# Performance work log

Hardware: AMD Instinct MI355X
Metric: run time of the kernel (lower is better)

Reference implementation:

```python
import jax, jax.numpy as jnp
import numpy as np

NEG = 0.2  # LeakyReLU slope

def lrelu(x):
    return jnp.where(x >= 0, x, NEG * x)

def conv2d(x, w, pad):
    return jax.lax.conv_general_dilated(x, w, (1, 1), [(pad, pad), (pad, pad)],
                                        dimension_numbers=('NCHW', 'OIHW', 'NCHW'))

def maxpool2(x):
    return jax.lax.reduce_window(x, -jnp.inf, jax.lax.max, (1, 1, 2, 2), (1, 1, 2, 2), 'VALID')

def batchnorm(x, g, b, eps=1e-5):
    m = jnp.mean(x, axis=(0, 2, 3), keepdims=True)
    v = jnp.var(x, axis=(0, 2, 3), keepdims=True)
    return (x - m) / jnp.sqrt(v + eps) * g[None, :, None, None] + b[None, :, None, None]

def features(x, cw1, bg1, bb1, cw2, bg2, bb2, cw3, bg3, bb3, cw4, bg4, bb4):
    x = maxpool2(lrelu(batchnorm(conv2d(x, cw1, 1), bg1, bb1)))
    x = maxpool2(lrelu(batchnorm(conv2d(x, cw2, 1), bg2, bb2)))
    x = lrelu(batchnorm(conv2d(x, cw3, 1), bg3, bb3))
    x = lrelu(batchnorm(conv2d(x, cw4, 1), bg4, bb4))
    return x  # [B,64,16,16]

def mhsa(x, wq, bq, wk, bk, wv, bv, rel_h, rel_w, ln_g, ln_b, heads=4):
    B, C, W, H = x.shape
    d, hw = C // heads, W * H
    def proj(w, b):
        return (jnp.einsum('oc,bchw->bohw', w, x) + b[None, :, None, None]).reshape(B, heads, d, hw)
    q, k, v = proj(wq, bq), proj(wk, bk), proj(wv, bv)
    cc = jnp.einsum('bhdi,bhdj->bhij', q, k)                 # content-content
    pos = (rel_h + rel_w).reshape(heads, d, hw)              # relative position bias
    cp = jnp.einsum('hdi,bhdj->bhij', pos, q)                # content-position
    attn = jax.nn.softmax(cc + cp, axis=-1)
    out = jnp.einsum('bhdj,bhij->bhdi', v, attn).reshape(B, C, W, H)
    m = jnp.mean(out, axis=(1, 2, 3), keepdims=True)
    va = jnp.var(out, axis=(1, 2, 3), keepdims=True)
    out = (out - m) / jnp.sqrt(va + 1e-5) * ln_g[None] + ln_b[None]
    return out + x

def cbam(x, cw1, cb1, cw2, cb2, sw, sb):
    avg, mx = jnp.mean(x, axis=(2, 3)), jnp.max(x, axis=(2, 3))
    def exc(f):
        return jnp.einsum('oc,bc->bo', cw2, jax.nn.relu(jnp.einsum('oc,bc->bo', cw1, f) + cb1)) + cb2
    x = jax.nn.sigmoid(exc(avg) + exc(mx))[:, :, None, None] * x
    sf = jnp.stack([jnp.mean(x, axis=1), jnp.max(x, axis=1)], axis=1)  # [B,2,H,W]
    sa = jax.nn.sigmoid(conv2d(sf, sw, 3) + sb[None, :, None, None])
    return sa * x

def sa_module(x, mh, cb):
    return mhsa(x, *mh) + cbam(x, *cb) + x

def setup_inputs() -> dict:
    key = jax.random.key(0)
    ks = jax.random.split(key, 24)
    rn = lambda k, s, sc=1.0: jax.random.normal(k, s, dtype=jnp.float32) * sc
    inp = {
        'input1': rn(ks[0], (64, 1, 64, 64)),
        'input2': rn(ks[1], (5, 5, 1, 64, 64)),
        'conv1_w': rn(ks[2], (64, 1, 3, 3), 0.3),
        'bn1_g': jnp.ones(64), 'bn1_b': jnp.zeros(64),
        'conv2_w': rn(ks[3], (64, 64, 3, 3), 0.05),
        'bn2_g': jnp.ones(64), 'bn2_b': jnp.zeros(64),
        'conv3_w': rn(ks[4], (64, 64, 3, 3), 0.05),
        'bn3_g': jnp.ones(64), 'bn3_b': jnp.zeros(64),
        'conv4_w': rn(ks[5], (64, 64, 3, 3), 0.05),
        'bn4_g': jnp.ones(64), 'bn4_b': jnp.zeros(64),
        'wq': rn(ks[6], (64, 64), 0.12), 'bq': rn(ks[7], (64,), 0.01),
        'wk': rn(ks[8], (64, 64), 0.12), 'bk': rn(ks[9], (64,), 0.01),
        'wv': rn(ks[10], (64, 64), 0.12), 'bv': rn(ks[11], (64,), 0.01),
        'rel_h': rn(ks[12], (1, 4, 16, 1, 16)),
        'rel_w': rn(ks[13], (1, 4, 16, 16, 1)),
        'ln_g': jnp.ones((64, 16, 16)), 'ln_b': jnp.zeros((64, 16, 16)),
        'ca_w1': rn(ks[14], (4, 64), 0.15), 'ca_b1': jnp.zeros(4),
        'ca_w2': rn(ks[15], (64, 4), 0.15), 'ca_b2': jnp.zeros(64),
        'sa_w': rn(ks[16], (1, 2, 7, 7), 0.1), 'sa_b': jnp.zeros(1),
        'cls_w': rn(ks[17], (256,), 0.05),
    }
    return inp

def reference(input1, input2, conv1_w, bn1_g, bn1_b, conv2_w, bn2_g, bn2_b,
              conv3_w, bn3_g, bn3_b, conv4_w, bn4_g, bn4_b,
              wq, bq, wk, bk, wv, bv, rel_h, rel_w, ln_g, ln_b,
              ca_w1, ca_b1, ca_w2, ca_b2, sa_w, sa_b, cls_w):
    fa = (conv1_w, bn1_g, bn1_b, conv2_w, bn2_g, bn2_b, conv3_w, bn3_g, bn3_b, conv4_w, bn4_g, bn4_b)
    mh = (wq, bq, wk, bk, wv, bv, rel_h, rel_w, ln_g, ln_b)
    cb = (ca_w1, ca_b1, ca_w2, ca_b2, sa_w, sa_b)
    q = sa_module(features(input1, *fa), mh, cb)                      # [B,64,16,16]
    S = jax.vmap(lambda imgs: sa_module(features(imgs, *fa), mh, cb))(input2)  # [ncls,shot,64,16,16]
    ncls, shot = input2.shape[0], input2.shape[1]
    B, C, Hh, Ww = q.shape
    hw = Hh * Ww
    # per-class covariance over channels (CovaBlock.cal_covariance)
    X = S.transpose(0, 2, 1, 3, 4).reshape(ncls, C, shot * hw)
    Xc = X - jnp.mean(X, axis=2, keepdims=True)
    cov = jnp.einsum('ncm,ndm->ncd', Xc, Xc) / (hw * shot - 1)        # [ncls,C,C]
    # query similarity: diag(q^T Cov q) done as fused quadratic form
    Q = q.reshape(B, C, hw)
    Qn = Q / jnp.linalg.norm(Q, axis=2, keepdims=True)
    sim = jnp.einsum('bci,jcd,bdi->bji', Qn, cov, Qn)                 # [B,ncls,hw]
    # classifier: LeakyReLU -> Dropout(eval=identity) -> Conv1d(k=hw, stride=hw, no bias)
    out = jnp.einsum('bjk,k->bj', lrelu(sim), cls_w)
    return out
```

## Files before the change

kernel.cpp:

```cpp
#include <hip/hip_runtime.h>
#include <hip/hip_bf16.h>

__device__ __forceinline__ float lrelu(float x){ return x >= 0.f ? x : 0.2f*x; }
__device__ __forceinline__ float sigm(float x){ return 1.f/(1.f+__expf(-x)); }

typedef short short8 __attribute__((ext_vector_type(8)));
typedef float f32x16 __attribute__((ext_vector_type(16)));

static constexpr size_t OFF_X0    = 0;
static constexpr size_t OFF_POS   = 475712;
static constexpr size_t OFF_WQT   = 492096;
static constexpr size_t OFF_STATS = 504384;
static constexpr size_t OFF_P1    = 507456;
static constexpr size_t OFF_P2    = 7092224;
static constexpr size_t OFF_S3    = 8937728;
static constexpr size_t OFF_S4    = 8943872;
static constexpr size_t OFF_WH3   = 8950016;
static constexpr size_t OFF_WL3   = 8968448;
static constexpr size_t OFF_WH4   = 8986880;
static constexpr size_t OFF_WL4   = 9005312;
static constexpr size_t OFF_S2    = 9023744;
static constexpr size_t OFF_RES   = 10714688;
static constexpr size_t OFF_MU    = 12172864;
static constexpr size_t OFF_COV   = 12173184;
static constexpr size_t OFF_SIM   = 12193664;
static constexpr size_t OFF_R1    = 12275584;
static constexpr size_t OFF_C2    = OFF_R1;
static constexpr size_t OFF_ATP   = OFF_R1;
static constexpr size_t OFF_C3    = OFF_R1 + 5832704;
static constexpr size_t OFF_C4    = OFF_R1 + 8749056;
static constexpr size_t OFF_CKV   = OFF_R1 + 10207232;
static constexpr size_t OFF_C3P   = OFF_R1 + 10207232;
static constexpr size_t OFF_QN    = OFF_R1 + 17543680;
static constexpr size_t OFF_WH    = OFF_R1 + 21737984;
static constexpr size_t OFF_WL    = OFF_WH + 18432;

__device__ __forceinline__ int bn_group(int img){ return (img < 64) ? 0 : (1 + (img-64)/5); }

__device__ __forceinline__ void bn_ab(const float* __restrict__ sums, int g, int c, float n,
                                      float gw, float bw, float& a, float& b)
{
    const float sum = sums[(g*64+c)*2], ss = sums[(g*64+c)*2+1];
    const float m = sum/n;
    const float var = fmaxf(ss/n - m*m, 0.f);
    const float istd = 1.f/sqrtf(var + 1e-5f);
    a = gw*istd;
    b = bw - m*a;
}

__device__ __forceinline__ void bn_ab_s8(const float* __restrict__ sums, int g, int c, float n,
                                         float gw, float bw, float& a, float& b)
{
    float sum = 0.f, ss = 0.f;
#pragma unroll
    for (int s=0;s<8;s++){
        sum += sums[s*768 + (g*64+c)*2];
        ss  += sums[s*768 + (g*64+c)*2 + 1];
    }
    const float m = sum/n;
    const float var = fmaxf(ss/n - m*m, 0.f);
    const float istd = 1.f/sqrtf(var + 1e-5f);
    a = gw*istd;
    b = bw - m*a;
}

__global__ __launch_bounds__(256) void prep_k(const float* __restrict__ in1, const float* __restrict__ in2,
        const float* __restrict__ relh, const float* __restrict__ relw,
        const float* __restrict__ wq, const float* __restrict__ wk, const float* __restrict__ wv,
        const float* __restrict__ cw2, const float* __restrict__ cw3, const float* __restrict__ cw4,
        float* __restrict__ ws)
{
    int idx = blockIdx.x*256 + threadIdx.x;
    if (idx < 364544) { ws[OFF_X0+idx] = (idx < 262144 ? in1[idx] : in2[idx-262144]); return; }
    idx -= 364544;
    if (idx < 16384) {
        const int h = idx>>12, r = idx&4095, i = r>>4, d = r&15;
        ws[OFF_POS+idx] = relh[h*256 + d*16 + (i&15)] + relw[h*256 + d*16 + (i>>4)];
        return;
    }
    idx -= 16384;
    if (idx < 12288) {
        const int s = idx/4096, r = idx%4096, c = r>>6, o = r&63;
        const float* wp = (s==0)?wq:((s==1)?wk:wv);
        ws[OFF_WQT+idx] = wp[o*64 + c];
        return;
    }
    idx -= 12288;
    if (idx < 3072) { ws[OFF_STATS+idx] = 0.f; return; }
    idx -= 3072;
    if (idx < 20480) { ws[OFF_COV+idx] = 0.f; return; }
    idx -= 20480;
    if (idx < 12288) { ws[OFF_S3+idx] = 0.f; return; }
    idx -= 12288;
    if (idx < 768) { ws[OFF_S2+idx] = 0.f; return; }
    idx -= 768;
    if (idx < 110592) {
        const int which = idx / 36864, r0 = idx - which*36864;
        const int och = r0/576, rr = r0%576, cin = rr/9, k9 = rr%9;
        const float* cwp = (which==0)?cw2:((which==1)?cw3:cw4);
        const float v = cwp[r0];
        __hip_bfloat16 hb = __float2bfloat16(v);
        const float hv = __bfloat162float(hb);
        __hip_bfloat16 lb = __float2bfloat16(v - hv);
        const size_t oh = (which==0)?OFF_WH:((which==1)?OFF_WH3:OFF_WH4);
        const size_t ol = (which==0)?OFF_WL:((which==1)?OFF_WL3:OFF_WL4);
        unsigned short* WH = (unsigned short*)(ws + oh);
        unsigned short* WL = (unsigned short*)(ws + ol);
        const int d = k9*4096 + och*64 + cin;
        WH[d] = *(unsigned short*)&hb;
        WL[d] = *(unsigned short*)&lb;
        return;
    }
    idx -= 110592;
    if (idx < 751872) {
        const int img = idx/8448, r = idx%8448;
        const int pos = r>>6, d = r&63;
        int ypad, xpad;
        if (pos < 68){ ypad = (pos<34)?0:33; xpad = (pos<34)?pos:(pos-34); }
        else { const int q = pos-68; ypad = 1 + (q>>1); xpad = (q&1)*33; }
        ws[OFF_P1 + (((size_t)img*34 + ypad)*34 + xpad)*64 + d] = 0.f;
        return;
    }
    idx -= 751872;
    if (idx < 387328) {
        const int img = idx/4352, r = idx%4352;
        const int pos = r>>6, d = r&63;
        int ypad, xpad;
        if (pos < 36){ ypad = (pos<18)?0:17; xpad = (pos<18)?pos:(pos-18); }
        else { const int q = pos-36; ypad = 1 + (q>>1); xpad = (q&1)*17; }
        ws[OFF_P2 + (((size_t)img*18 + ypad)*18 + xpad)*64 + d] = 0.f;
        return;
    }
    idx -= 387328;
    if (idx < 387328) {
        const int img = idx/4352, r = idx%4352;
        const int pos = r>>6, d = r&63;
        int ypad, xpad;
        if (pos < 36){ ypad = (pos<18)?0:17; xpad = (pos<18)?pos:(pos-18); }
        else { const int q = pos-36; ypad = 1 + (q>>1); xpad = (q&1)*17; }
        ws[OFF_C3P + (((size_t)img*18 + ypad)*18 + xpad)*64 + d] = 0.f;
    }
}

template<int H, int W, int CIN, int CH, int OCB, int PT, bool STORE, bool INBN>
__global__ __launch_bounds__(256) void conv3x3_k(const float* __restrict__ in,
                                                 const float* __restrict__ wt,
                                                 float* __restrict__ out,
                                                 float* __restrict__ bnsum,
                                                 const float* __restrict__ isums,
                                                 const float* __restrict__ igw,
                                                 const float* __restrict__ ibw,
                                                 int ihw)
{
    constexpr int P = W + 1;
    constexpr int PLANE = H * P;
    constexpr int HW = H * W;
    constexpr int PASSES = HW / (256 * PT);
    constexpr int NLD = CH * HW / 256;
    __shared__ float lds[CH * PLANE];
    __shared__ float redS[OCB*4], redQ[OCB*4];
    __shared__ float abA[64], abB[64];
    const int img = blockIdx.x;
    const int och0 = blockIdx.y * OCB;
    const int t = threadIdx.x;

    if constexpr (INBN) {
        if (t < CIN) {
            const int gi = bn_group(img);
            const float nin = (float)(((gi==0)?64:5) * ihw);
            float a, b;
            bn_ab(isums, gi, t, nin, igw[t], ibw[t], a, b);
            abA[t]=a; abB[t]=b;
        }
        __syncthreads();
    }

    float acc[PASSES][OCB][PT];
#pragma unroll
    for (int a=0;a<PASSES;a++)
#pragma unroll
      for (int o=0;o<OCB;o++)
#pragma unroll
        for (int p=0;p<PT;p++) acc[a][o][p]=0.f;

    for (int idx = t; idx < CH*HW; idx += 256) {
        const int c = idx / HW, p = idx % HW;
        float v = in[((size_t)img*CIN + c)*HW + p];
        if constexpr (INBN) v = lrelu(abA[c]*v + abB[c]);
        lds[c*PLANE + (p/W)*P + (p%W)] = v;
    }
    __syncthreads();

    for (int cc0 = 0; cc0 < CIN; cc0 += CH) {
        float pre[(CIN > CH) ? NLD : 1];
        if constexpr (CIN > CH) {
            if (cc0 + CH < CIN) {
#pragma unroll
                for (int j=0;j<NLD;j++){
                    const int idx = j*256 + t;
                    const int c = idx / HW, p = idx % HW;
                    pre[j] = in[((size_t)img*CIN + cc0 + CH + c)*HW + p];
                }
            }
        }
        for (int c = 0; c < CH; ++c) {
            float wr[OCB][9];
#pragma unroll
            for (int o=0;o<OCB;o++)
#pragma unroll
              for (int k=0;k<9;k++)
                wr[o][k] = wt[((size_t)(och0+o)*CIN + (cc0+c))*9 + k];
            const float* Lc = lds + c*PLANE;
#pragma unroll
            for (int ps=0; ps<PASSES; ++ps) {
                const int px0 = (ps*256 + t)*PT;
                const int y = px0 / W, x0 = px0 % W;
#pragma unroll
                for (int ky=0; ky<3; ++ky) {
                    const int yy = y + ky - 1;
                    if (yy >= 0 && yy < H) {
                        const float* Lr = Lc + yy*P;
                        float r[PT+2];
                        r[0] = (x0 > 0) ? Lr[x0-1] : 0.f;
#pragma unroll
                        for (int k2=0;k2<PT;k2++) r[k2+1] = Lr[x0+k2];
                        r[PT+1] = (x0+PT < W) ? Lr[x0+PT] : 0.f;
#pragma unroll
                        for (int p=0;p<PT;p++)
#pragma unroll
                          for (int kx=0;kx<3;kx++) {
                              const float v = r[p+kx];
#pragma unroll
                              for (int o=0;o<OCB;o++)
                                  acc[ps][o][p] += v * wr[o][ky*3+kx];
                          }
                    }
                }
            }
        }
        if constexpr (CIN > CH) {
            if (cc0 + CH < CIN) {
                __syncthreads();
#pragma unroll
                for (int j=0;j<NLD;j++){
                    const int idx = j*256 + t;
                    const int c = idx / HW, p = idx % HW;
                    float v = pre[j];
                    if constexpr (INBN) v = lrelu(abA[cc0+CH+c]*v + abB[cc0+CH+c]);
                    lds[c*PLANE + (p/W)*P + (p%W)] = v;
                }
                __syncthreads();
            }
        }
    }
    if constexpr (STORE) {
#pragma unroll
        for (int ps=0; ps<PASSES; ++ps) {
            const int px0 = (ps*256 + t)*PT;
#pragma unroll
            for (int o=0;o<OCB;o++)
#pragma unroll
              for (int p=0;p<PT;p++)
                out[((size_t)img*64 + och0+o)*HW + px0 + p] = acc[ps][o][p];
        }
    }
    const int g = bn_group(img);
    const int wv = t >> 6;
#pragma unroll
    for (int o=0;o<OCB;o++){
        float s=0.f, ss=0.f;
#pragma unroll
        for (int ps=0;ps<PASSES;ps++)
#pragma unroll
          for (int p=0;p<PT;p++){ const float v=acc[ps][o][p]; s+=v; ss+=v*v; }
#pragma unroll
        for (int off=32; off>0; off>>=1){ s += __shfl_xor(s, off); ss += __shfl_xor(ss, off); }
        if ((t&63)==0){ redS[o*4+wv]=s; redQ[o*4+wv]=ss; }
    }
    __syncthreads();
    if (t < OCB*2){
        const int o = t>>1, metric = t&1;
        const float v = metric ? (redQ[o*4]+redQ[o*4+1]+redQ[o*4+2]+redQ[o*4+3])
                               : (redS[o*4]+redS[o*4+1]+redS[o*4+2]+redS[o*4+3]);
        atomicAdd(&bnsum[(g*64 + och0+o)*2 + metric], v);
    }
}

__global__ __launch_bounds__(256) void bnpoolconv1_k(const float* __restrict__ x0,
        const float* __restrict__ cw, const float* __restrict__ sums,
        const float* __restrict__ gw, const float* __restrict__ bw,
        unsigned short* __restrict__ p1p)
{
    __shared__ float xl[10*64];
    __shared__ float wsm[576];
    __shared__ float aAs[64], aBs[64];
    const int img = blockIdx.x, band = blockIdx.y, t = threadIdx.x;
    const int oy0 = band*4;
    const float* xp = x0 + (size_t)img*4096;
    for (int idx=t; idx<640; idx+=256){
        const int iy = idx>>6, ix = idx&63;
        const int gy = 2*oy0 - 1 + iy;
        xl[idx] = (gy>=0 && gy<64) ? xp[gy*64+ix] : 0.f;
    }
    const int g = bn_group(img);
    if (t < 64){
        const float n = (float)(((g==0)?64:5) * 4096);
        float a, b;
        bn_ab(sums, g, t, n, gw[t], bw[t], a, b);
        aAs[t]=a; aBs[t]=b;
    }
    for (int idx=t; idx<576; idx+=256) wsm[idx] = cw[idx];
    __syncthreads();
    const int p = t>>1, half = t&1;
    const int ly = p>>5, ox = p&31;
    float r[4][4];
#pragma unroll
    for (int dy=0;dy<4;dy++){
        const float* Lr = xl + (2*ly+dy)*64;
#pragma unroll
        for (int dx=0;dx<4;dx++){
            const int xx = 2*ox-1+dx;
            r[dy][dx] = (xx>=0 && xx<64) ? Lr[xx] : 0.f;
        }
    }
    short8 hv[4], lv[4];
#pragma unroll
    for (int o=0;o<32;o++){
        const int och = half*32 + o;
        float w[9];
#pragma unroll
        for (int k=0;k<9;k++) w[k] = wsm[och*9+k];
        const float a = aAs[och], b = aBs[och];
        float best = -1e30f;
#pragma unroll
        for (int sy=0;sy<2;sy++)
#pragma unroll
          for (int sx=0;sx<2;sx++){
            float s=0.f;
#pragma unroll
            for (int ky=0;ky<3;ky++)
#pragma unroll
              for (int kx=0;kx<3;kx++) s += r[sy+ky][sx+kx]*w[ky*3+kx];
            best = fmaxf(best, lrelu(a*s+b));
          }
        __hip_bfloat16 hb = __float2bfloat16(best);
        const float hf = __bfloat162float(hb);
        __hip_bfloat16 lb = __float2bfloat16(best - hf);
        hv[o>>3][o&7] = (short)*(unsigned short*)&hb;
        lv[o>>3][o&7] = (short)*(unsigned short*)&lb;
    }
    const size_t base = ((((size_t)img*34 + (oy0+ly) + 1)*34) + ox + 1)*128 + half*32;
#pragma unroll
    for (int j=0;j<4;j++){
        *(short8*)(p1p + base + j*8)      = hv[j];
        *(short8*)(p1p + base + 64 + j*8) = lv[j];
    }
}

__global__ __launch_bounds__(256) void conv2mfma_k(const unsigned short* __restrict__ p1p,
        const unsigned short* __restrict__ whi, const unsigned short* __restrict__ wlo,
        float* __restrict__ c2)
{
    __shared__ __align__(16) unsigned short Bx[136*128];
    const int img = blockIdx.x, rowblk = blockIdx.y;
    const int t = threadIdx.x;
    {
        const unsigned short* src = p1p + (((size_t)img*34 + rowblk*2)*34)*128;
        for (int idx=t; idx<2176; idx+=256){
            const int pos = idx>>4, sub = idx&15;
            const short8 v = *(const short8*)(src + pos*128 + sub*8);
            *(short8*)(Bx + pos*128 + ((sub ^ (pos&15))<<3)) = v;
        }
    }
    __syncthreads();
    const int lane = t & 63, wv = t >> 6;
    const int mt = wv & 1, ntp = wv >> 1;
    const int m = lane & 31, kg = lane >> 5;
    f32x16 accA, accB, accC;
#pragma unroll
    for (int r=0;r<16;r++){ accA[r]=0.f; accB[r]=0.f; accC[r]=0.f; }

#pragma unroll
    for (int ky=0; ky<3; ky++){
#pragma unroll
      for (int kx=0; kx<3; kx++){
        const int s = ky*3 + kx;
        const unsigned short* wh = whi + ((s*64 + mt*32 + m)<<6) + kg*8;
        const unsigned short* wl = wlo + ((s*64 + mt*32 + m)<<6) + kg*8;
        const int pos = (ntp+ky)*34 + m + kx;
        const int pb  = pos << 7;
        const int sw  = (pos & 15) << 3;
#pragma unroll
        for (int ch=0; ch<4; ch++){
            const int o = ch*16 + (kg<<3);
            const short8 ah = *(const short8*)(wh + ch*16);
            const short8 al = *(const short8*)(wl + ch*16);
            const short8 bh = *(const short8*)(Bx + pb + (o ^ sw));
            const short8 bl = *(const short8*)(Bx + pb + ((64 + o) ^ sw));
            accA = __builtin_amdgcn_mfma_f32_32x32x16_bf16(ah, bh, accA, 0,0,0);
            accB = __builtin_amdgcn_mfma_f32_32x32x16_bf16(al, bh, accB, 0,0,0);
            accC = __builtin_amdgcn_mfma_f32_32x32x16_bf16(ah, bl, accC, 0,0,0);
        }
      }
    }
    const int py = rowblk*2 + ntp;
    float* co = c2 + (size_t)img*65536 + py*32 + m;
#pragma unroll
    for (int r=0; r<16; r++){
        const int och = mt*32 + (r&3) + 8*(r>>2) + 4*kg;
        co[(size_t)och*1024] = accA[r] + accB[r] + accC[r];
    }
}

__global__ __launch_bounds__(256) void bnstats2_k(const float* __restrict__ in, float* __restrict__ sums)
{
    __shared__ float rs[4], rq[4];
    const int img = blockIdx.x, c = blockIdx.y, t = threadIdx.x;
    const float4 v = ((const float4*)(in + ((size_t)img*64 + c)*1024))[t];
    float s = v.x+v.y+v.z+v.w;
    float q = v.x*v.x+v.y*v.y+v.z*v.z+v.w*v.w;
#pragma unroll
    for (int off=32; off>0; off>>=1){ s += __shfl_xor(s, off); q += __shfl_xor(q, off); }
    if ((t&63)==0){ rs[t>>6]=s; rq[t>>6]=q; }
    __syncthreads();
    if (t==0){
        const int g = bn_group(img);
        atomicAdd(&sums[(g*64+c)*2],   rs[0]+rs[1]+rs[2]+rs[3]);
        atomicAdd(&sums[(g*64+c)*2+1], rq[0]+rq[1]+rq[2]+rq[3]);
    }
}

__global__ __launch_bounds__(256) void bnpool_pack_k(const float* __restrict__ c2,
        const float* __restrict__ sums, const float* __restrict__ gw, const float* __restrict__ bw,
        unsigned short* __restrict__ p2p)
{
    __shared__ float aA[64], aB[64];
    const int img = blockIdx.x, cb = blockIdx.y, t = threadIdx.x;
    const int g = bn_group(img);
    if (t < 64){
        const float n = (float)(((g==0)?64:5) * 1024);
        float a, b;
        bn_ab(sums, g, t, n, gw[t], bw[t], a, b);
        aA[t]=a; aB[t]=b;
    }
    __syncthreads();
    const int oy = t>>4, ox = t&15;
    const float* pim = c2 + (size_t)img*65536 + (size_t)cb*32768 + oy*64 + ox*2;
    short8 hv[4], lv[4];
#pragma unroll
    for (int j8=0;j8<4;j8++){
#pragma unroll
      for (int e=0;e<8;e++){
        const int j = j8*8 + e;
        const int c = cb*32 + j;
        const float* pl = pim + (size_t)j*1024;
        const float2 u = *(const float2*)pl;
        const float2 v = *(const float2*)(pl + 32);
        const float a = aA[c], b = aB[c];
        const float best = fmaxf(fmaxf(lrelu(a*u.x+b), lrelu(a*u.y+b)),
                                 fmaxf(lrelu(a*v.x+b), lrelu(a*v.y+b)));
        __hip_bfloat16 hb = __float2bfloat16(best);
        const float hf = __bfloat162float(hb);
        __hip_bfloat16 lb = __float2bfloat16(best - hf);
        hv[j8][e] = (short)*(unsigned short*)&hb;
        lv[j8][e] = (short)*(unsigned short*)&lb;
      }
    }
    unsigned short* dst = p2p + (((size_t)img*18 + oy+1)*18 + ox+1)*128 + cb*32;
#pragma unroll
    for (int j=0;j<4;j++){
        *(short8*)(dst + j*8)      = hv[j];
        *(short8*)(dst + 64 + j*8) = lv[j];
    }
}

__global__ __launch_bounds__(256) void conv16mfma_k(const unsigned short* __restrict__ pack,
        const unsigned short* __restrict__ whi, const unsigned short* __restrict__ wlo,
        float* __restrict__ out, float* __restrict__ bnsum)
{
    __shared__ __align__(16) unsigned short Bx[108*128];
    const int img = blockIdx.x, rowblk = blockIdx.y;
    const int t = threadIdx.x;
    {
        const unsigned short* src = pack + (((size_t)img*18 + rowblk*4)*18)*128;
        for (int idx=t; idx<1728; idx+=256){
            const int pos = idx>>4, sub = idx&15;
            const short8 v = *(const short8*)(src + pos*128 + sub*8);
            *(short8*)(Bx + pos*128 + ((sub ^ (pos&15))<<3)) = v;
        }
    }
    __syncthreads();
    const int lane = t & 63, wv = t >> 6;
    const int mt = wv & 1, np = wv >> 1;
    const int m = lane & 31, kg = lane >> 5;
    f32x16 accA, accB, accC;
#pragma unroll
    for (int r=0;r<16;r++){ accA[r]=0.f; accB[r]=0.f; accC[r]=0.f; }

#pragma unroll
    for (int ky=0; ky<3; ky++){
#pragma unroll
      for (int kx=0; kx<3; kx++){
        const int s = ky*3 + kx;
        const unsigned short* wh = whi + ((s*64 + mt*32 + m)<<6) + kg*8;
        const unsigned short* wl = wlo + ((s*64 + mt*32 + m)<<6) + kg*8;
        const int pos = (np*2 + (m>>4) + ky)*18 + (m&15) + kx;
        const int pb  = pos << 7;
        const int sw  = (pos & 15) << 3;
#pragma unroll
        for (int ch=0; ch<4; ch++){
            const int o = ch*16 + (kg<<3);
            const short8 ah = *(const short8*)(wh + ch*16);
            const short8 al = *(const short8*)(wl + ch*16);
            const short8 bh = *(const short8*)(Bx + pb + (o ^ sw));
            const short8 bl = *(const short8*)(Bx + pb + ((64 + o) ^ sw));
            accA = __builtin_amdgcn_mfma_f32_32x32x16_bf16(ah, bh, accA, 0,0,0);
            accB = __builtin_amdgcn_mfma_f32_32x32x16_bf16(al, bh, accB, 0,0,0);
            accC = __builtin_amdgcn_mfma_f32_32x32x16_bf16(ah, bl, accC, 0,0,0);
        }
      }
    }
    float* co = out + (size_t)img*16384 + rowblk*64 + np*32 + m;
    float fa[16];
#pragma unroll
    for (int r=0; r<16; r++){
        fa[r] = accA[r] + accB[r] + accC[r];
        const int och = mt*32 + (r&3) + 8*(r>>2) + 4*kg;
        co[(size_t)och*256] = fa[r];
    }
    const int g = bn_group(img);
    float* bs = bnsum + (rowblk*2 + np)*768;
#pragma unroll
    for (int r=0; r<16; r++){
        float sv = fa[r], qv = fa[r]*fa[r];
#pragma unroll
        for (int off=16; off>0; off>>=1){ sv += __shfl_xor(sv, off); qv += __shfl_xor(qv, off); }
        if (m == r){
            const int och = mt*32 + (r&3) + 8*(r>>2) + 4*kg;
            atomicAdd(&bs[(g*64+och)*2],   sv);
            atomicAdd(&bs[(g*64+och)*2+1], qv);
        }
    }
}

__global__ __launch_bounds__(256) void c3pack_k(const float* __restrict__ c3,
        const float* __restrict__ s3, const float* __restrict__ gw, const float* __restrict__ bw,
        unsigned short* __restrict__ c3p)
{
    __shared__ float aA[64], aB[64];
    const int img = blockIdx.x, cb = blockIdx.y, t = threadIdx.x;
    const int g = bn_group(img);
    if (t < 64){
        const float n = (float)(((g==0)?64:5) * 256);
        float a, b;
        bn_ab_s8(s3, g, t, n, gw[t], bw[t], a, b);
        aA[t]=a; aB[t]=b;
    }
    __syncthreads();
    const float* pim = c3 + (size_t)img*16384 + (size_t)cb*8192 + t;
    short8 hv[4], lv[4];
#pragma unroll
    for (int j8=0;j8<4;j8++){
#pragma unroll
      for (int e=0;e<8;e++){
        const int j = j8*8 + e;
        const int c = cb*32 + j;
        const float v = lrelu(aA[c]*pim[(size_t)j*256] + aB[c]);
        __hip_bfloat16 hb = __float2bfloat16(v);
        const float hf = __bfloat162float(hb);
        __hip_bfloat16 lb = __float2bfloat16(v - hf);
        hv[j8][e] = (short)*(unsigned short*)&hb;
        lv[j8][e] = (short)*(unsigned short*)&lb;
      }
    }
    const int oy = t>>4, ox = t&15;
    unsigned short* dst = c3p + (((size_t)img*18 + oy+1)*18 + ox+1)*128 + cb*32;
#pragma unroll
    for (int j=0;j<4;j++){
        *(short8*)(dst + j*8)      = hv[j];
        *(short8*)(dst + 64 + j*8) = lv[j];
    }
}

__global__ __launch_bounds__(256) void proj_k(const float* __restrict__ c4, const float* __restrict__ wT,
               const float* __restrict__ bq, const float* __restrict__ bk, const float* __restrict__ bv,
               const float* __restrict__ sums4, const float* __restrict__ gw4, const float* __restrict__ bw4,
               float* __restrict__ ckv)
{
    __shared__ float xl[64*256];
    const int img = blockIdx.x, s = blockIdx.y, t = threadIdx.x;
    const int gi = bn_group(img);
    const float nin = (float)(((gi==0)?64:5) * 256);
    {
        const float4* in4 = (const float4*)(c4 + (size_t)img*16384);
        float4* xl4 = (float4*)xl;
        for (int i=t; i<4096; i+=256){
            float4 v = in4[i];
            const int c = i>>6;
            float a, b;
            bn_ab_s8(sums4, gi, c, nin, gw4[c], bw4[c], a, b);
            v.x=lrelu(a*v.x+b); v.y=lrelu(a*v.y+b); v.z=lrelu(a*v.z+b); v.w=lrelu(a*v.w+b);
            xl4[i] = v;
        }
    }
    const float* bias = (s==0)?bq:((s==1)?bk:bv);
    const int sofs = (s==0)?16:((s==1)?0:32);
    const float* wp = wT + s*4096;
    const int o0 = (t>>4)*4, i0 = (t&15)*16;
    const int h = o0>>4, d0 = o0&15;
    __syncthreads();
    float acc[4][16];
    float b0[4];
#pragma unroll
// ... 205 lines not shown
#pragma unroll 4
        for (int cc=0; cc<16; ++cc){
            const int c = cb*16 + cc;
            const int i4 = c*64 + q;
            const float4 mv = *(const float4*)&mh_l[c*256 + q*4];
            const float4 fv = fb4[i4], gv = lg4[i4], bv = lb4[i4];
            const float a = aA[c], b = aB[c], cf = ca[c];
            float4 r;
            r.x = (mv.x-m)*istd*gv.x + bv.x + lrelu(a*fv.x+b)*(2.f + sa0*cf);
            r.y = (mv.y-m)*istd*gv.y + bv.y + lrelu(a*fv.y+b)*(2.f + sa1*cf);
            r.z = (mv.z-m)*istd*gv.z + bv.z + lrelu(a*fv.z+b)*(2.f + sa2*cf);
            r.w = (mv.w-m)*istd*gv.w + bv.w + lrelu(a*fv.w+b)*(2.f + sa3*cf);
            res4[i4] = r;
        }
    }
}

__global__ __launch_bounds__(256) void covmu_k(const float* __restrict__ res, float* __restrict__ mu)
{
    __shared__ float r1[256];
    const int n = blockIdx.x, c = blockIdx.y, t = threadIdx.x;
    float s=0.f;
    for (int sh=0; sh<5; ++sh)
        s += res[((size_t)(64 + n*5 + sh)*64 + c)*256 + t];
    r1[t]=s; __syncthreads();
    for (int st=128;st>0;st>>=1){ if(t<st) r1[t]+=r1[t+st]; __syncthreads(); }
    if (t==0) mu[n*64+c] = r1[0]/1280.f;
}

__global__ __launch_bounds__(256) void cov_k(const float* __restrict__ res, const float* __restrict__ mu,
                                             float* __restrict__ cov)
{
    __shared__ float Xl[64*129];
    const int n = blockIdx.x, by = blockIdx.y, sh = blockIdx.z, t = threadIdx.x;
    const int c = by*16 + (t>>4);
    const int d0 = (t&15)*4;
    float acc[4] = {0.f,0.f,0.f,0.f};
    for (int half=0; half<2; ++half){
        __syncthreads();
        for (int idx=t; idx<8192; idx+=256){
            const int ch = idx>>7, p = idx&127;
            Xl[ch*129+p] = res[((size_t)(64+n*5+sh)*64 + ch)*256 + half*128 + p] - mu[n*64+ch];
        }
        __syncthreads();
        for (int p=0;p<128;p++){
            const float xc = Xl[c*129+p];
#pragma unroll
            for (int k=0;k<4;k++) acc[k] += xc*Xl[(d0+k)*129+p];
        }
    }
#pragma unroll
    for (int k=0;k<4;k++) atomicAdd(&cov[((size_t)n*64 + c)*64 + d0+k], acc[k]*(1.f/1279.f));
}

__global__ __launch_bounds__(64) void qn_k(const float* __restrict__ res, float* __restrict__ qn)
{
    const int b = blockIdx.x, c = blockIdx.y, t = threadIdx.x;
    const size_t base = ((size_t)b*64 + c)*256;
    const float4 v = *(const float4*)(res + base + t*4);
    float ss = v.x*v.x + v.y*v.y + v.z*v.z + v.w*v.w;
#pragma unroll
    for (int off=32; off>0; off>>=1) ss += __shfl_xor(ss, off);
    const float inv = 1.f/sqrtf(ss);
    float4 o; o.x=v.x*inv; o.y=v.y*inv; o.z=v.z*inv; o.w=v.w*inv;
    *(float4*)(qn + base + t*4) = o;
}

__global__ __launch_bounds__(256) void sim_k(const float* __restrict__ qn, const float* __restrict__ cov,
                                             float* __restrict__ sim)
{
    __shared__ float covj[64*65];
    __shared__ float Vl[64*68];
    __shared__ float simred[320];
    const int b = blockIdx.x, iq = blockIdx.y, t = threadIdx.x;
    const int i0g = iq*64;
    for (int idx=t; idx<4096; idx+=256){
        const int c = idx>>6, il = idx&63;
        Vl[c*68+il] = qn[((size_t)b*64+c)*256 + i0g + il];
    }
    for (int idx=t; idx<320; idx+=256) simred[idx]=0.f;
    const int c0 = (t>>4)*4, i0 = (t&15)*4;
    for (int j=0;j<5;j++){
        __syncthreads();
        for (int idx=t; idx<4096; idx+=256)
            covj[(idx>>6)*65 + (idx&63)] = cov[(size_t)j*4096 + idx];
        __syncthreads();
        float pt[4][4];
#pragma unroll
        for (int a=0;a<4;a++)
#pragma unroll
          for (int bb=0;bb<4;bb++) pt[a][bb]=0.f;
        for (int d=0; d<64; ++d){
            const float4 vv = *(const float4*)&Vl[d*68 + i0];
            float cw[4];
#pragma unroll
            for (int cc=0;cc<4;cc++) cw[cc] = covj[(c0+cc)*65 + d];
#pragma unroll
            for (int cc=0;cc<4;cc++){
                pt[cc][0] += cw[cc]*vv.x;
                pt[cc][1] += cw[cc]*vv.y;
                pt[cc][2] += cw[cc]*vv.z;
                pt[cc][3] += cw[cc]*vv.w;
            }
        }
#pragma unroll
        for (int ii=0;ii<4;ii++){
            float s = 0.f;
#pragma unroll
            for (int cc=0;cc<4;cc++) s += pt[cc][ii]*Vl[(c0+cc)*68 + i0+ii];
            atomicAdd(&simred[j*64 + i0 + ii], s);
        }
    }
    __syncthreads();
    for (int idx=t; idx<320; idx+=256){
        const int j = idx>>6, il = idx&63;
        sim[((size_t)b*5 + j)*256 + i0g + il] = simred[idx];
    }
}

__global__ __launch_bounds__(256) void cls_k(const float* __restrict__ sim, const float* __restrict__ cw,
                                             float* __restrict__ out)
{
    __shared__ float red[256];
    const int b = blockIdx.x, t = threadIdx.x;
    const float w = cw[t];
    for (int j=0;j<5;j++){
        const float v = sim[((size_t)b*5 + j)*256 + t];
        red[t] = lrelu(v)*w;
        __syncthreads();
        for (int st=128;st>0;st>>=1){ if(t<st) red[t]+=red[t+st]; __syncthreads(); }
        if (t==0) out[b*5+j] = red[0];
        __syncthreads();
    }
}

extern "C" void kernel_launch(void* const* d_in, const int* in_sizes, int n_in,
                              void* d_out, int out_size, void* d_ws, size_t ws_size,
                              hipStream_t stream)
{
    const float* IN[31];
    for (int i=0;i<31;i++) IN[i] = (const float*)d_in[i];
    float* W = (float*)d_ws;
    float* OUT = (float*)d_out;
    const unsigned short* WHp  = (const unsigned short*)(W + OFF_WH);
    const unsigned short* WLp  = (const unsigned short*)(W + OFF_WL);
    const unsigned short* WH3p = (const unsigned short*)(W + OFF_WH3);
    const unsigned short* WL3p = (const unsigned short*)(W + OFF_WL3);
    const unsigned short* WH4p = (const unsigned short*)(W + OFF_WH4);
    const unsigned short* WL4p = (const unsigned short*)(W + OFF_WL4);
    unsigned short* P1P = (unsigned short*)(W + OFF_P1);
    unsigned short* P2P = (unsigned short*)(W + OFF_P2);
    unsigned short* C3P = (unsigned short*)(W + OFF_C3P);

    prep_k<<<8074,256,0,stream>>>(IN[0],IN[1],IN[20],IN[21],IN[14],IN[16],IN[18],
                                  IN[5],IN[8],IN[11],W);

    conv3x3_k<64,64,1,1,4,4,false,false><<<dim3(89,16),256,0,stream>>>(W+OFF_X0, IN[2], nullptr, W+OFF_STATS, nullptr,nullptr,nullptr,0);
    bnpoolconv1_k<<<dim3(89,8),256,0,stream>>>(W+OFF_X0, IN[2], W+OFF_STATS, IN[3], IN[4], P1P);

    conv2mfma_k<<<dim3(89,16),256,0,stream>>>(P1P, WHp, WLp, W+OFF_C2);
    bnstats2_k<<<dim3(89,64),256,0,stream>>>(W+OFF_C2, W+OFF_S2);
    bnpool_pack_k<<<dim3(89,2),256,0,stream>>>(W+OFF_C2, W+OFF_S2, IN[6], IN[7], P2P);

    conv16mfma_k<<<dim3(89,4),256,0,stream>>>(P2P, WH3p, WL3p, W+OFF_C3, W+OFF_S3);
    c3pack_k<<<dim3(89,2),256,0,stream>>>(W+OFF_C3, W+OFF_S3, IN[9], IN[10], C3P);

    conv16mfma_k<<<dim3(89,4),256,0,stream>>>(C3P, WH4p, WL4p, W+OFF_C4, W+OFF_S4);

    proj_k<<<dim3(89,3),256,0,stream>>>(W+OFF_C4, W+OFF_WQT, IN[15], IN[17], IN[19],
                                        W+OFF_S4, IN[12], IN[13], W+OFF_CKV);
    attnp_k<<<dim3(89,4,4),256,0,stream>>>(W+OFF_CKV, W+OFF_POS, W+OFF_ATP);

    post_k<<<89,256,0,stream>>>(W+OFF_ATP, IN[22], IN[23], W+OFF_C4,
                                W+OFF_S4, IN[12], IN[13],
                                IN[24], IN[25], IN[26], IN[27], IN[28], IN[29], W+OFF_RES);

    covmu_k<<<dim3(5,64),256,0,stream>>>(W+OFF_RES, W+OFF_MU);
    cov_k<<<dim3(5,4,5),256,0,stream>>>(W+OFF_RES, W+OFF_MU, W+OFF_COV);
    qn_k<<<dim3(64,64),64,0,stream>>>(W+OFF_RES, W+OFF_QN);
    sim_k<<<dim3(64,4),256,0,stream>>>(W+OFF_QN, W+OFF_COV, W+OFF_SIM);
    cls_k<<<64,256,0,stream>>>(W+OFF_SIM, IN[30], OUT);
}
```

Before: 512.1 us.

## Fuse conv2 BN statistics and 2x2 max/min pooling into the MFMA conv epilogue

The conv2 MFMA kernel now reduces per-channel sum and sum-of-squares with wave shuffles and atomics into 32 slot-partitioned accumulators. It also pools 2x2 windows into max and min buffers, so the full 32x32 conv2 output is never written to global memory. The separate bnstats2 kernel is removed. bnpool_pack picks max or min depending on the sign of the BN scale, which stays exact because lrelu is monotone. This removes a large intermediate write and read plus a launch, at the cost of more atomics and extra epilogue work in the conv kernel.

```diff
diff --git a/kernel.cpp b/kernel.cpp
--- a/kernel.cpp
+++ b/kernel.cpp
@@ -25,7 +25,8 @@
 static constexpr size_t OFF_COV   = 12173184;
 static constexpr size_t OFF_SIM   = 12193664;
 static constexpr size_t OFF_R1    = 12275584;
-static constexpr size_t OFF_C2    = OFF_R1;
+static constexpr size_t OFF_PMAX  = OFF_R1;
+static constexpr size_t OFF_PMIN  = OFF_R1 + 1458176;
 static constexpr size_t OFF_ATP   = OFF_R1;
 static constexpr size_t OFF_C3    = OFF_R1 + 5832704;
 static constexpr size_t OFF_C4    = OFF_R1 + 8749056;
@@ -64,6 +65,22 @@
     b = bw - m*a;
 }
 
+__device__ __forceinline__ void bn_ab_s32(const float* __restrict__ sums, int g, int c, float n,
+                                          float gw, float bw, float& a, float& b)
+{
+    float sum = 0.f, ss = 0.f;
+#pragma unroll
+    for (int s=0;s<32;s++){
+        sum += sums[s*768 + (g*64+c)*2];
+        ss  += sums[s*768 + (g*64+c)*2 + 1];
+    }
+    const float m = sum/n;
+    const float var = fmaxf(ss/n - m*m, 0.f);
+    const float istd = 1.f/sqrtf(var + 1e-5f);
+    a = gw*istd;
+    b = bw - m*a;
+}
+
 __global__ __launch_bounds__(256) void prep_k(const float* __restrict__ in1, const float* __restrict__ in2,
         const float* __restrict__ relh, const float* __restrict__ relw,
         const float* __restrict__ wq, const float* __restrict__ wk, const float* __restrict__ wv,
@@ -92,8 +109,8 @@
     idx -= 20480;
     if (idx < 12288) { ws[OFF_S3+idx] = 0.f; return; }
     idx -= 12288;
-    if (idx < 768) { ws[OFF_S2+idx] = 0.f; return; }
-    idx -= 768;
+    if (idx < 24576) { ws[OFF_S2+idx] = 0.f; return; }
+    idx -= 24576;
     if (idx < 110592) {
         const int which = idx / 36864, r0 = idx - which*36864;
         const int och = r0/576, rr = r0%576, cin = rr/9, k9 = rr%9;
@@ -359,7 +376,7 @@
 
 __global__ __launch_bounds__(256) void conv2mfma_k(const unsigned short* __restrict__ p1p,
         const unsigned short* __restrict__ whi, const unsigned short* __restrict__ wlo,
-        float* __restrict__ c2)
+        float* __restrict__ pmax, float* __restrict__ pmin, float* __restrict__ bnsum)
 {
     __shared__ __align__(16) unsigned short Bx[136*128];
     const int img = blockIdx.x, rowblk = blockIdx.y;
@@ -403,34 +420,54 @@
         }
       }
     }
-    const int py = rowblk*2 + ntp;
-    float* co = c2 + (size_t)img*65536 + py*32 + m;
+    float fa[16];
+#pragma unroll
+    for (int r=0;r<16;r++) fa[r] = accA[r] + accB[r] + accC[r];
+
+    const int g = bn_group(img);
+    float* bs = bnsum + (rowblk*2 + ntp)*768;
+#pragma unroll
+    for (int r=0; r<16; r++){
+        float sv = fa[r], qv = fa[r]*fa[r];
+#pragma unroll
+        for (int off=16; off>0; off>>=1){ sv += __shfl_xor(sv, off); qv += __shfl_xor(qv, off); }
+        if (m == r){
+            const int och = mt*32 + (r&3) + 8*(r>>2) + 4*kg;
+            atomicAdd(&bs[(g*64+och)*2],   sv);
+            atomicAdd(&bs[(g*64+och)*2+1], qv);
+        }
+    }
+
+    __syncthreads();
+    float* Bxf = (float*)Bx;
 #pragma unroll
     for (int r=0; r<16; r++){
         const int och = mt*32 + (r&3) + 8*(r>>2) + 4*kg;
-        co[(size_t)och*1024] = accA[r] + accB[r] + accC[r];
-    }
-}
-
-__global__ __launch_bounds__(256) void bnstats2_k(const float* __restrict__ in, float* __restrict__ sums)
-{
-    __shared__ float rs[4], rq[4];
-    const int img = blockIdx.x, c = blockIdx.y, t = threadIdx.x;
-    const float4 v = ((const float4*)(in + ((size_t)img*64 + c)*1024))[t];
-    float s = v.x+v.y+v.z+v.w;
-    float q = v.x*v.x+v.y*v.y+v.z*v.z+v.w*v.w;
-#pragma unroll
-    for (int off=32; off>0; off>>=1){ s += __shfl_xor(s, off); q += __shfl_xor(q, off); }
-    if ((t&63)==0){ rs[t>>6]=s; rq[t>>6]=q; }
-    __syncthreads();
-    if (t==0){
-        const int g = bn_group(img);
-        atomicAdd(&sums[(g*64+c)*2],   rs[0]+rs[1]+rs[2]+rs[3]);
-        atomicAdd(&sums[(g*64+c)*2+1], rq[0]+rq[1]+rq[2]+rq[3]);
-    }
-}
-
-__global__ __launch_bounds__(256) void bnpool_pack_k(const float* __restrict__ c2,
+        Bxf[(ntp*64 + och)*32 + m] = fa[r];
+    }
+    __syncthreads();
+    {
+        const int och = t>>2;
+        const int j0 = (t&3)*4;
+        const float* r0 = Bxf + och*32;
+        const float* r1 = Bxf + (64+och)*32;
+        float4 mxv, mnv;
+        float* mxp = (float*)&mxv; float* mnp = (float*)&mnv;
+#pragma unroll
+        for (int k=0;k<4;k++){
+            const int j = j0+k;
+            const float a0 = r0[2*j], a1 = r0[2*j+1], b0 = r1[2*j], b1 = r1[2*j+1];
+            mxp[k] = fmaxf(fmaxf(a0,a1), fmaxf(b0,b1));
+            mnp[k] = fminf(fminf(a0,a1), fminf(b0,b1));
+        }
+        const size_t base = ((size_t)img*64 + och)*256 + rowblk*16 + j0;
+        *(float4*)(pmax + base) = mxv;
+        *(float4*)(pmin + base) = mnv;
+    }
+}
+
+__global__ __launch_bounds__(256) void bnpool_pack_k(const float* __restrict__ pmax,
+        const float* __restrict__ pmin,
         const float* __restrict__ sums, const float* __restrict__ gw, const float* __restrict__ bw,
         unsigned short* __restrict__ p2p)
 {
@@ -440,12 +477,11 @@
     if (t < 64){
         const float n = (float)(((g==0)?64:5) * 1024);
         float a, b;
-        bn_ab(sums, g, t, n, gw[t], bw[t], a, b);
+        bn_ab_s32(sums, g, t, n, gw[t], bw[t], a, b);
         aA[t]=a; aB[t]=b;
     }
     __syncthreads();
     const int oy = t>>4, ox = t&15;
-    const float* pim = c2 + (size_t)img*65536 + (size_t)cb*32768 + oy*64 + ox*2;
     short8 hv[4], lv[4];
 #pragma unroll
     for (int j8=0;j8<4;j8++){
@@ -453,12 +489,10 @@
       for (int e=0;e<8;e++){
         const int j = j8*8 + e;
         const int c = cb*32 + j;
-        const float* pl = pim + (size_t)j*1024;
-        const float2 u = *(const float2*)pl;
-        const float2 v = *(const float2*)(pl + 32);
         const float a = aA[c], b = aB[c];
-        const float best = fmaxf(fmaxf(lrelu(a*u.x+b), lrelu(a*u.y+b)),
-                                 fmaxf(lrelu(a*v.x+b), lrelu(a*v.y+b)));
+        const size_t o = ((size_t)img*64 + c)*256 + t;
+        const float x = (a >= 0.f) ? pmax[o] : pmin[o];
+        const float best = lrelu(a*x + b);
         __hip_bfloat16 hb = __float2bfloat16(best);
         const float hf = __bfloat162float(hb);
         __hip_bfloat16 lb = __float2bfloat16(best - hf);
@@ -970,15 +1004,14 @@
     unsigned short* P2P = (unsigned short*)(W + OFF_P2);
     unsigned short* C3P = (unsigned short*)(W + OFF_C3P);
 
-    prep_k<<<8074,256,0,stream>>>(IN[0],IN[1],IN[20],IN[21],IN[14],IN[16],IN[18],
+    prep_k<<<8167,256,0,stream>>>(IN[0],IN[1],IN[20],IN[21],IN[14],IN[16],IN[18],
                                   IN[5],IN[8],IN[11],W);
 
     conv3x3_k<64,64,1,1,4,4,false,false><<<dim3(89,16),256,0,stream>>>(W+OFF_X0, IN[2], nullptr, W+OFF_STATS, nullptr,nullptr,nullptr,0);
     bnpoolconv1_k<<<dim3(89,8),256,0,stream>>>(W+OFF_X0, IN[2], W+OFF_STATS, IN[3], IN[4], P1P);
 
-    conv2mfma_k<<<dim3(89,16),256,0,stream>>>(P1P, WHp, WLp, W+OFF_C2);
-    bnstats2_k<<<dim3(89,64),256,0,stream>>>(W+OFF_C2, W+OFF_S2);
-    bnpool_pack_k<<<dim3(89,2),256,0,stream>>>(W+OFF_C2, W+OFF_S2, IN[6], IN[7], P2P);
+    conv2mfma_k<<<dim3(89,16),256,0,stream>>>(P1P, WHp, WLp, W+OFF_PMAX, W+OFF_PMIN, W+OFF_S2);
+    bnpool_pack_k<<<dim3(89,2),256,0,stream>>>(W+OFF_PMAX, W+OFF_PMIN, W+OFF_S2, IN[6], IN[7], P2P);
 
     conv16mfma_k<<<dim3(89,4),256,0,stream>>>(P2P, WH3p, WL3p, W+OFF_C3, W+OFF_S3);
     c3pack_k<<<dim3(89,2),256,0,stream>>>(W+OFF_C3, W+OFF_S3, IN[9], IN[10], C3P);
```

After: 511.6 us. No clear change (-0.1%).

## Fuse conv2 BN statistics and 2x2 max/min pooling into MFMA epilogue

Applied to the files above, without the earlier changes.

The conv2 MFMA kernel now stages its output tile in shared memory and writes per-block BN partial sums plus pooled 2x2 max and min values, instead of the full pre-pool activation. A small deterministic reduction kernel replaces the atomic-based stats kernel. The pool/pack kernel picks the max or min depending on the sign of the BN scale, since the affine-plus-LeakyReLU map is monotone. This removes one full write and two full reads of the conv2 activation, at the cost of an extra shared-memory pass and barriers in the conv epilogue.

```diff
diff --git a/kernel.cpp b/kernel.cpp
--- a/kernel.cpp
+++ b/kernel.cpp
@@ -19,13 +19,14 @@
 static constexpr size_t OFF_WL3   = 8968448;
 static constexpr size_t OFF_WH4   = 8986880;
 static constexpr size_t OFF_WL4   = 9005312;
-static constexpr size_t OFF_S2    = 9023744;
+static constexpr size_t OFF_PBS   = 9023744;
+static constexpr size_t OFF_S2    = 9206016;
 static constexpr size_t OFF_RES   = 10714688;
 static constexpr size_t OFF_MU    = 12172864;
 static constexpr size_t OFF_COV   = 12173184;
 static constexpr size_t OFF_SIM   = 12193664;
 static constexpr size_t OFF_R1    = 12275584;
-static constexpr size_t OFF_C2    = OFF_R1;
+static constexpr size_t OFF_PMM   = OFF_R1;
 static constexpr size_t OFF_ATP   = OFF_R1;
 static constexpr size_t OFF_C3    = OFF_R1 + 5832704;
 static constexpr size_t OFF_C4    = OFF_R1 + 8749056;
@@ -92,8 +93,6 @@
     idx -= 20480;
     if (idx < 12288) { ws[OFF_S3+idx] = 0.f; return; }
     idx -= 12288;
-    if (idx < 768) { ws[OFF_S2+idx] = 0.f; return; }
-    idx -= 768;
     if (idx < 110592) {
         const int which = idx / 36864, r0 = idx - which*36864;
         const int och = r0/576, rr = r0%576, cin = rr/9, k9 = rr%9;
@@ -359,7 +358,7 @@
 
 __global__ __launch_bounds__(256) void conv2mfma_k(const unsigned short* __restrict__ p1p,
         const unsigned short* __restrict__ whi, const unsigned short* __restrict__ wlo,
-        float* __restrict__ c2)
+        float* __restrict__ pmm, float* __restrict__ pbs)
 {
     __shared__ __align__(16) unsigned short Bx[136*128];
     const int img = blockIdx.x, rowblk = blockIdx.y;
@@ -403,34 +402,67 @@
         }
       }
     }
-    const int py = rowblk*2 + ntp;
-    float* co = c2 + (size_t)img*65536 + py*32 + m;
+    float fa[16];
+#pragma unroll
+    for (int r=0;r<16;r++) fa[r] = accA[r] + accB[r] + accC[r];
+
+    __syncthreads();
+    float* Bxf = (float*)Bx;
 #pragma unroll
     for (int r=0; r<16; r++){
         const int och = mt*32 + (r&3) + 8*(r>>2) + 4*kg;
-        co[(size_t)och*1024] = accA[r] + accB[r] + accC[r];
-    }
-}
-
-__global__ __launch_bounds__(256) void bnstats2_k(const float* __restrict__ in, float* __restrict__ sums)
-{
-    __shared__ float rs[4], rq[4];
-    const int img = blockIdx.x, c = blockIdx.y, t = threadIdx.x;
-    const float4 v = ((const float4*)(in + ((size_t)img*64 + c)*1024))[t];
-    float s = v.x+v.y+v.z+v.w;
-    float q = v.x*v.x+v.y*v.y+v.z*v.z+v.w*v.w;
-#pragma unroll
-    for (int off=32; off>0; off>>=1){ s += __shfl_xor(s, off); q += __shfl_xor(q, off); }
-    if ((t&63)==0){ rs[t>>6]=s; rq[t>>6]=q; }
-    __syncthreads();
-    if (t==0){
-        const int g = bn_group(img);
-        atomicAdd(&sums[(g*64+c)*2],   rs[0]+rs[1]+rs[2]+rs[3]);
-        atomicAdd(&sums[(g*64+c)*2+1], rq[0]+rq[1]+rq[2]+rq[3]);
-    }
-}
-
-__global__ __launch_bounds__(256) void bnpool_pack_k(const float* __restrict__ c2,
+        Bxf[(ntp*64 + och)*33 + m] = fa[r];
+    }
+    __syncthreads();
+    {
+        const int och = t>>2, q4 = t&3;
+        const int c0 = q4*8;
+        const float* r0 = Bxf + och*33 + c0;
+        const float* r1 = Bxf + (64+och)*33 + c0;
+        float4 mxv, mnv;
+        float* mxp = (float*)&mxv; float* mnp = (float*)&mnv;
+        float s = 0.f, q = 0.f;
+#pragma unroll
+        for (int k=0;k<4;k++){
+            const float a0 = r0[2*k], a1 = r0[2*k+1], b0 = r1[2*k], b1 = r1[2*k+1];
+            mxp[k] = fmaxf(fmaxf(a0,a1), fmaxf(b0,b1));
+            mnp[k] = fminf(fminf(a0,a1), fminf(b0,b1));
+            s += a0+a1+b0+b1;
+            q += a0*a0+a1*a1+b0*b0+b1*b1;
+        }
+        float* base = pmm + (((size_t)img*64 + och)*16 + rowblk)*32;
+        *(float4*)(base + q4*4)      = mxv;
+        *(float4*)(base + 16 + q4*4) = mnv;
+        s += __shfl_xor(s, 1); q += __shfl_xor(q, 1);
+        s += __shfl_xor(s, 2); q += __shfl_xor(q, 2);
+        if (q4 == 0){
+            float* pb = pbs + (size_t)(img*16 + rowblk)*128 + och*2;
+            pb[0] = s; pb[1] = q;
+        }
+    }
+}
+
+__global__ __launch_bounds__(256) void bnred_k(const float* __restrict__ pbs, float* __restrict__ sums)
+{
+    __shared__ float rs[256], rq[256];
+    const int g = blockIdx.x, t = threadIdx.x;
+    const int c = t & 63, qtr = t >> 6;
+    const int i0 = (g==0) ? 0 : (64 + (g-1)*5);
+    const int nslots = ((g==0)?64:5) * 16;
+    float s=0.f, q=0.f;
+    for (int sl = qtr; sl < nslots; sl += 4){
+        const float* p = pbs + (size_t)(i0*16 + sl)*128 + c*2;
+        s += p[0]; q += p[1];
+    }
+    rs[t]=s; rq[t]=q;
+    __syncthreads();
+    if (t < 64){
+        sums[(g*64+c)*2]   = rs[c]+rs[64+c]+rs[128+c]+rs[192+c];
+        sums[(g*64+c)*2+1] = rq[c]+rq[64+c]+rq[128+c]+rq[192+c];
+    }
+}
+
+__global__ __launch_bounds__(256) void bnpool_pack_k(const float* __restrict__ pmm,
         const float* __restrict__ sums, const float* __restrict__ gw, const float* __restrict__ bw,
         unsigned short* __restrict__ p2p)
 {
@@ -445,7 +477,6 @@
     }
     __syncthreads();
     const int oy = t>>4, ox = t&15;
-    const float* pim = c2 + (size_t)img*65536 + (size_t)cb*32768 + oy*64 + ox*2;
     short8 hv[4], lv[4];
 #pragma unroll
     for (int j8=0;j8<4;j8++){
@@ -453,12 +484,9 @@
       for (int e=0;e<8;e++){
         const int j = j8*8 + e;
         const int c = cb*32 + j;
-        const float* pl = pim + (size_t)j*1024;
-        const float2 u = *(const float2*)pl;
-        const float2 v = *(const float2*)(pl + 32);
         const float a = aA[c], b = aB[c];
-        const float best = fmaxf(fmaxf(lrelu(a*u.x+b), lrelu(a*u.y+b)),
-                                 fmaxf(lrelu(a*v.x+b), lrelu(a*v.y+b)));
+        const size_t o = (((size_t)img*64 + c)*16 + oy)*32 + ox + (a >= 0.f ? 0 : 16);
+        const float best = lrelu(a*pmm[o] + b);
         __hip_bfloat16 hb = __float2bfloat16(best);
         const float hf = __bfloat162float(hb);
         __hip_bfloat16 lb = __float2bfloat16(best - hf);
@@ -970,15 +998,15 @@
     unsigned short* P2P = (unsigned short*)(W + OFF_P2);
     unsigned short* C3P = (unsigned short*)(W + OFF_C3P);
 
-    prep_k<<<8074,256,0,stream>>>(IN[0],IN[1],IN[20],IN[21],IN[14],IN[16],IN[18],
+    prep_k<<<8071,256,0,stream>>>(IN[0],IN[1],IN[20],IN[21],IN[14],IN[16],IN[18],
                                   IN[5],IN[8],IN[11],W);
 
     conv3x3_k<64,64,1,1,4,4,false,false><<<dim3(89,16),256,0,stream>>>(W+OFF_X0, IN[2], nullptr, W+OFF_STATS, nullptr,nullptr,nullptr,0);
     bnpoolconv1_k<<<dim3(89,8),256,0,stream>>>(W+OFF_X0, IN[2], W+OFF_STATS, IN[3], IN[4], P1P);
 
-    conv2mfma_k<<<dim3(89,16),256,0,stream>>>(P1P, WHp, WLp, W+OFF_C2);
-    bnstats2_k<<<dim3(89,64),256,0,stream>>>(W+OFF_C2, W+OFF_S2);
-    bnpool_pack_k<<<dim3(89,2),256,0,stream>>>(W+OFF_C2, W+OFF_S2, IN[6], IN[7], P2P);
+    conv2mfma_k<<<dim3(89,16),256,0,stream>>>(P1P, WHp, WLp, W+OFF_PMM, W+OFF_PBS);
+    bnred_k<<<6,256,0,stream>>>(W+OFF_PBS, W+OFF_S2);
+    bnpool_pack_k<<<dim3(89,2),256,0,stream>>>(W+OFF_PMM, W+OFF_S2, IN[6], IN[7], P2P);
 
     conv16mfma_k<<<dim3(89,4),256,0,stream>>>(P2P, WH3p, WL3p, W+OFF_C3, W+OFF_S3);
     c3pack_k<<<dim3(89,2),256,0,stream>>>(W+OFF_C3, W+OFF_S3, IN[9], IN[10], C3P);
```

Result: slower. 553.6 us (+8.1%).
